# Kernel tuning notes

Hardware: AMD Instinct MI355X
Metric: run time of the kernel (lower is better)

The kernel has to match this reference:

```python
import jax, jax.numpy as jnp
import numpy as np

# SLAYER neuron / simulation constants (from params)
THETA = 10.0      # spike threshold
TAU_SR = 10.0     # PSP (synaptic response) time constant
TS = 1.0          # simulation time step
TAU_RHO = 1.0     # surrogate-gradient width
SCALE_RHO = 1.0   # surrogate-gradient scale
ALPHA = float(np.exp(-TS / TAU_SR))  # leaky-filter decay per step

B, C_IN, T = 32, 156, 2048
HID, OUT = 512, 20


@jax.custom_vjp
def spike(u):
    # Hard threshold with SLAYER-style exponential surrogate gradient.
    return (u >= THETA).astype(u.dtype)

def _spike_fwd(u):
    return spike(u), u

def _spike_bwd(u, g):
    sg = (SCALE_RHO / TAU_RHO) * jnp.exp(-jnp.abs(u - THETA) / TAU_RHO)
    return (g * sg,)

spike.defvjp(_spike_fwd, _spike_bwd)


def psp(x):
    # Leaky exponential temporal filter along the LAST axis (SLAYER psp):
    # y[t] = ALPHA * y[t-1] + x[t]
    xt = jnp.moveaxis(x, -1, 0)  # [T, ...]
    def step(c, xi):
        c = ALPHA * c + xi
        return c, c
    _, y = jax.lax.scan(step, jnp.zeros_like(xt[0]), xt)
    return jnp.moveaxis(y, 0, -1)


def dense(x, W):
    # SLAYER dense layer: per-timestep fully-connected over channel dim.
    # x: [N, C, H, W, T], W: [O, C] -> [N, O, H, W, T]
    return jnp.einsum('oc,nchwt->nohwt', W, x)


def _make_perm():
    rng = np.random.default_rng(0)
    random_list = rng.permutation(np.arange(1, 40))
    perm = []
    for i in random_list:
        perm.append(2 * int(i) - 2)
        perm.append(2 * int(i) - 1)
    for i in random_list:
        perm.append(2 * int(i) - 2 + 78)
        perm.append(2 * int(i) - 1 + 78)
    return jnp.asarray(perm, dtype=jnp.int32)


def setup_inputs() -> dict:
    key = jax.random.key(0)
    k0, k1, k2, k3, k4 = jax.random.split(key, 5)
    spike_input = jax.random.randint(k0, (B, C_IN, 1, 1, T), 0, 2).astype(jnp.float32)
    W1 = jax.random.normal(k1, (HID, C_IN), dtype=jnp.float32) * (C_IN ** -0.5)
    W2 = jax.random.normal(k2, (OUT, HID), dtype=jnp.float32) * (HID ** -0.5)
    Wl1 = jax.random.normal(k3, (HID, T), dtype=jnp.float32) * (T ** -0.5)
    Wl2 = jax.random.normal(k4, (OUT, HID), dtype=jnp.float32) * (HID ** -0.5)
    perm = _make_perm()
    return {"spike_input": spike_input, "W1": W1, "W2": W2,
            "Wl1": Wl1, "Wl2": Wl2, "perm": perm}


def reference(spike_input, W1, W2, Wl1, Wl2, perm):
    # Branch 1: channel-dense over taxels, PSP + spike, twice.
    s1 = spike(psp(dense(spike_input, W1)))          # [B, HID, 1, 1, T]
    spike_output = spike(psp(dense(s1, W2)))         # [B, OUT, 1, 1, T]

    # Branch 2: transpose channel<->time, permute taxel axis, dense over time dim.
    x_t = jnp.swapaxes(spike_input, 1, 4)            # [B, T, 1, 1, C_IN]
    x_tp = x_t[..., perm]                            # gather on taxel axis
    l1 = spike(psp(dense(x_tp, Wl1)))                # [B, HID, 1, 1, C_IN]
    location_output = spike(psp(dense(l1, Wl2)))     # [B, OUT, 1, 1, C_IN]

    return jnp.concatenate([spike_output, location_output], axis=4)
```

## Files before the change

kernel.cpp:

```cpp
#include <hip/hip_runtime.h>

#define ALPHA  0.90483741803595952f
#define ALPHA8 0.44932896411722156f
#define A64C   5.82e-23f
#define THETA  10.0f
#define BF1    ((unsigned short)0x3F80)
#define ISCALE 0.015625f

typedef short   bf16x8 __attribute__((ext_vector_type(8)));
typedef float   f32x4  __attribute__((ext_vector_type(4)));
typedef float   f32x4v __attribute__((ext_vector_type(4)));
typedef unsigned short ushort4v __attribute__((ext_vector_type(4)));
typedef unsigned short ushort8v __attribute__((ext_vector_type(8)));
typedef unsigned char  uchar4v  __attribute__((ext_vector_type(4)));
typedef unsigned char  uchar8v  __attribute__((ext_vector_type(8)));
typedef long long i64;

#define DMA16(gsrc, ldst)                                                     \
    __builtin_amdgcn_global_load_lds(                                         \
        (const __attribute__((address_space(1))) unsigned int*)(gsrc),        \
        (__attribute__((address_space(3))) unsigned int*)(ldst), 16, 0, 0)

__device__ __forceinline__ i64 tr16(const unsigned char* p) {
    i64 r;
    asm volatile("ds_read_b64_tr_b16 %0, %1"
                 : "=v"(r)
                 : "v"((const __attribute__((address_space(3))) unsigned char*)p));
    return r;
}

__device__ __forceinline__ unsigned short f2bf(float f) {
    unsigned int x = __float_as_uint(f);
    unsigned int r = (x + 0x7FFFu + ((x >> 16) & 1u)) >> 16;
    return (unsigned short)r;
}
__device__ __forceinline__ float bf2f(unsigned short h) {
    return __uint_as_float(((unsigned int)h) << 16);
}
__device__ __forceinline__ void split2(float w, unsigned short& h0,
                                       unsigned short& h1) {
    h0 = f2bf(w);          float r0 = w - bf2f(h0);
    h1 = f2bf(r0);
}
__device__ __forceinline__ unsigned char f2fp8(float f) {
    int pk = __builtin_amdgcn_cvt_pk_fp8_f32(f, 0.f, 0, false);
    return (unsigned char)(pk & 0xFF);
}
__device__ __forceinline__ float fp82f(unsigned char b) {
    return __builtin_amdgcn_cvt_f32_fp8((int)b, 0);
}

__global__ __launch_bounds__(256) void prep_scan_pack(
    const float* __restrict__ In, unsigned char* __restrict__ Infp8,
    unsigned short* __restrict__ Pbf,
    const float* __restrict__ W1,  const float* __restrict__ W2,
    const float* __restrict__ Wl1, const float* __restrict__ Wl2,
    unsigned short* __restrict__ W1p,  unsigned char* __restrict__ W2p8,
    unsigned char* __restrict__ Wl1p8, unsigned short* __restrict__ Wl2p)
{
    const int blk = blockIdx.x;
    const int tid = threadIdx.x;
    if (blk >= 6080) {
        int idx = blk - 6080;
        int b = idx >> 2, c = 156 + (idx & 3);
        ushort8v z = {0,0,0,0,0,0,0,0};
        *(ushort8v*)(Pbf + (long long)(b * 160 + c) * 2048 + tid * 8) = z;
        return;
    }
    if (blk < 1088) {
        if (blk < 512) {
            int m = blk;
            for (int k = tid; k < 2048; k += 256) {
                float w = Wl1[(long long)m * 2048 + k] * 64.0f;
                unsigned char h0 = f2fp8(w);
                unsigned char h1 = f2fp8(w - fp82f(h0));
                Wl1p8[(long long)m * 2048 + k] = h0;
                Wl1p8[1048576 + (long long)m * 2048 + k] = h1;
            }
        } else if (blk < 1024) {
            int m = blk - 512;
            for (int k = tid; k < 160; k += 256) {
                float v = (k < 156) ? W1[(long long)m * 156 + k] : 0.f;
                unsigned short h0, h1;
                split2(v, h0, h1);
                W1p[(long long)m * 160 + k] = h0;
                W1p[81920 + (long long)m * 160 + k] = h1;
            }
        } else if (blk < 1056) {
            int m = blk - 1024;
            for (int k = tid; k < 512; k += 256) {
                float w = (m < 20) ? W2[(long long)m * 512 + k] : 0.f;
                unsigned char h0 = f2fp8(w);
                unsigned char h1 = f2fp8(w - fp82f(h0));
                W2p8[(long long)m * 512 + k] = h0;
                W2p8[16384 + (long long)m * 512 + k] = h1;
            }
        } else {
            int m = blk - 1056;
            for (int k = tid; k < 512; k += 256) {
                float v = (m < 20) ? Wl2[(long long)m * 512 + k] : 0.f;
                unsigned short h0, h1;
                split2(v, h0, h1);
                Wl2p[(long long)m * 512 + k] = h0;
                Wl2p[16384 + (long long)m * 512 + k] = h1;
            }
        }
        return;
    }

    const int row = blk - 1088;
    const int bN  = row / 156;
    const int prow = bN * 160 + (row - bN * 156);
    const float* x = In + (long long)row * 2048 + tid * 8;
    const unsigned char ONE8 = f2fp8(1.0f);

    float v[8];
    *(f32x4v*)&v[0] = *(const f32x4v*)x;
    *(f32x4v*)&v[4] = *(const f32x4v*)(x + 4);

    uchar8v raw;
    #pragma unroll
    for (int k = 0; k < 8; ++k) raw[k] = (v[k] >= 0.5f) ? ONE8 : (unsigned char)0;
    *(uchar8v*)(Infp8 + (long long)row * 2048 + tid * 8) = raw;

    float y = 0.f;
    #pragma unroll
    for (int k = 0; k < 8; ++k) { y = ALPHA * y + v[k]; v[k] = y; }

    const int lane = tid & 63, wid = tid >> 6;
    float val = y, mm = ALPHA8;
    #pragma unroll
    for (int d = 1; d < 64; d <<= 1) {
        float p = __shfl_up(val, d);
        if (lane >= d) val += mm * p;
        mm *= mm;
    }
    __shared__ float wsum[4];
    if (lane == 63) wsum[wid] = val;
    __syncthreads();
    float pw = 0.f;
    #pragma unroll
    for (int w2 = 0; w2 < 3; ++w2)
        if (w2 < wid) pw = pw * A64C + wsum[w2];
    float prev = __shfl_up(val, 1);
    float a8l  = __expf(-0.8f * (float)lane);
    float carry = (lane == 0) ? pw : (prev + a8l * pw);

    ushort8v pv;
    float ak = ALPHA;
    #pragma unroll
    for (int k = 0; k < 8; ++k) {
        float yk = v[k] + ak * carry;
        ak *= ALPHA;
        pv[k] = f2bf(yk);
    }
    *(ushort8v*)(Pbf + (long long)prow * 2048 + tid * 8) = pv;
}

__global__ __launch_bounds__(256) void mega_gemm1(
    const unsigned short* __restrict__ W1p,
    const unsigned short* __restrict__ Pbf,
    unsigned short* __restrict__ S1bits,
    const unsigned char* __restrict__ Wl1p8,
    const unsigned char* __restrict__ Infp8,
    unsigned short* __restrict__ Zp)
{
    __shared__ alignas(16) unsigned char SMEM[49152];
    const int bx  = blockIdx.x;
    const int tid = threadIdx.x;
    const int lane = tid & 63, w = tid >> 6;
    const int wy = w >> 1, wx = w & 1;
    const int l15 = lane & 15, kq = lane >> 4;
    const int key = (l15 >> 1) & 3;

    if (bx >= 160) {
        unsigned char* Ab = SMEM;
        unsigned char* Bb = SMEM + 32768;

        const int id1 = bx - 160;
        const int z  = id1 >> 6;
        const int m0 = ((id1 >> 4) & 3) * 128;
        const int n0 = (id1 & 15) * 128;

        const unsigned short* gA[4]; int ldsA[4];
        #pragma unroll
        for (int s = 0; s < 4; ++s) {
            int id = tid + s * 256;
            int pl = id >> 9, m = (id >> 2) & 127, g = id & 3;
            int gs = g ^ ((m >> 1) & 3);
            gA[s] = W1p + (long long)pl * 81920 + (long long)(m0 + m) * 160 + gs * 8;
            ldsA[s] = id * 16;
        }
        const unsigned short* gB[2];
        #pragma unroll
        for (int s = 0; s < 2; ++s) {
            int id = tid + s * 256;
            int c  = ((id >> 6) << 2) | ((id >> 1) & 3);
            int t8 = ((((id >> 3) & 7) << 1) | (id & 1)) << 3;
            gB[s] = Pbf + (long long)(z * 160 + c) * 2048 + n0 + t8;
        }

        auto dmaA = [&](int buf) {
            unsigned char* dst = Ab + buf * 16384;
            #pragma unroll
            for (int s = 0; s < 4; ++s) { DMA16(gA[s], dst + ldsA[s]); gA[s] += 32; }
        };
        auto dmaB = [&](int buf) {
            unsigned char* dst = Bb + buf * 8192;
            #pragma unroll
            for (int s = 0; s < 2; ++s) {
                DMA16(gB[s], dst + (tid + s * 256) * 16);
                gB[s] += 65536;
            }
        };

        int aOff[2][4];
        #pragma unroll
        for (int pl = 0; pl < 2; ++pl)
            #pragma unroll
            for (int mt = 0; mt < 4; ++mt)
                aOff[pl][mt] = pl * 8192 + (wy * 64 + mt * 16 + l15) * 64 +
                               ((kq ^ key) * 16);
        const int bTr = wx * 512 + kq * 1920;

        f32x4 acc[4][4] = {};

        dmaA(0); dmaB(0);
        __syncthreads();

        #pragma unroll
        for (int it = 0; it < 5; ++it) {
            const int cur = it & 1;
            if (it < 4) { dmaA(cur ^ 1); dmaB(cur ^ 1); }

            const unsigned char* Ac = Ab + cur * 16384;
            const unsigned char* vB = Bb + cur * 8192 + bTr;
            bf16x8 bfr[4];
            #pragma unroll
            for (int nt = 0; nt < 4; ++nt) {
                union { i64 q[2]; bf16x8 v; } u;
                u.q[0] = tr16(vB + nt * 128);
                u.q[1] = tr16(vB + 1024 + nt * 128);
                bfr[nt] = u.v;
            }
            asm volatile("s_waitcnt lgkmcnt(0)" ::: "memory");
            __builtin_amdgcn_sched_barrier(0);

            #pragma unroll
            for (int pl = 0; pl < 2; ++pl) {
                #pragma unroll
                for (int mt = 0; mt < 4; ++mt) {
                    bf16x8 afr = *(const bf16x8*)(Ac + aOff[pl][mt]);
                    #pragma unroll
                    for (int nt = 0; nt < 4; ++nt)
                        acc[mt][nt] = __builtin_amdgcn_mfma_f32_16x16x32_bf16(
                            afr, bfr[nt], acc[mt][nt], 0, 0, 0);
                }
            }
            __syncthreads();
        }

        unsigned short* Db = S1bits + (long long)z * 512 * 128;
        #pragma unroll
        for (int mt = 0; mt < 4; ++mt) {
            #pragma unroll
            for (int i = 0; i < 4; ++i) {
                int m = m0 + wy * 64 + mt * 16 + kq * 4 + i;
                #pragma unroll
                for (int nt = 0; nt < 4; ++nt) {
                    unsigned long long mask = __ballot(acc[mt][nt][i] >= THETA);
                    if (l15 == 0) {
                        int nchunk = (n0 + wx * 64 + nt * 16) >> 4;
                        Db[(long long)nchunk * 512 + m] =
                            (unsigned short)((mask >> (kq * 16)) & 0xFFFFu);
                    }
                }
            }
        }
    } else {
        unsigned char* Ab = SMEM;
        unsigned char* Bb = SMEM + 32768;

        const int id0 = bx;
        const int nIdx = id0 % 40;
        if (nIdx >= 39) return;
        const int rest = id0 / 40;
        const int n0  = nIdx * 128;
        const int m0  = rest * 128;

        const unsigned char* gA8[4]; int ldsA8[4];
        #pragma unroll
        for (int s = 0; s < 4; ++s) {
            int id = tid + s * 256;
            int pl = id >> 9, m = (id >> 2) & 127, g = id & 3;
            int gs = g ^ ((m >> 1) & 3);
            gA8[s] = Wl1p8 + (long long)pl * 1048576 +
                     (long long)(m0 + m) * 2048 + gs * 16;
            ldsA8[s] = id * 16;
        }
        const unsigned char* gB8[2]; int ldsB8[2];
        #pragma unroll
        for (int s = 0; s < 2; ++s) {
            int id = tid + s * 256;
            int n = id >> 2, g = id & 3;
            int gs = g ^ ((n >> 1) & 3);
            gB8[s] = Infp8 + (long long)(n0 + n) * 2048 + gs * 16;
            ldsB8[s] = id * 16;
        }

        auto dmaA8 = [&](int buf) {
            unsigned char* dst = Ab + buf * 16384;
            #pragma unroll
            for (int s = 0; s < 4; ++s) { DMA16(gA8[s], dst + ldsA8[s]); gA8[s] += 64; }
        };
        auto dmaB8 = [&](int buf) {
            unsigned char* dst = Bb + buf * 8192;
            #pragma unroll
            for (int s = 0; s < 2; ++s) { DMA16(gB8[s], dst + ldsB8[s]); gB8[s] += 64; }
        };

        int aO8[2][4][2], bO8[4][2];
        #pragma unroll
        for (int ks = 0; ks < 2; ++ks) {
            const int gl = ks * 2 + (kq >> 1);
            const int sub = ((gl ^ key) * 16) + (kq & 1) * 8;
            #pragma unroll
            for (int pl = 0; pl < 2; ++pl)
                #pragma unroll
                for (int mt = 0; mt < 4; ++mt)
                    aO8[pl][mt][ks] = pl * 8192 +
                        (wy * 64 + mt * 16 + l15) * 64 + sub;
            #pragma unroll
            for (int nt = 0; nt < 4; ++nt)
                bO8[nt][ks] = (wx * 64 + nt * 16 + l15) * 64 + sub;
        }

        f32x4 acc[4][4] = {};

        dmaA8(0); dmaB8(0);
        __syncthreads();

        for (int it = 0; it < 32; ++it) {
            const int cur = it & 1;
            if (it < 31) { dmaA8(cur ^ 1); dmaB8(cur ^ 1); }

            const unsigned char* Ac = Ab + cur * 16384;
            const unsigned char* Bc = Bb + cur * 8192;
            #pragma unroll
            for (int ks = 0; ks < 2; ++ks) {
                i64 bfr[4];
                #pragma unroll
                for (int nt = 0; nt < 4; ++nt)
                    bfr[nt] = *(const i64*)(Bc + bO8[nt][ks]);
                #pragma unroll
                for (int pl = 0; pl < 2; ++pl) {
                    #pragma unroll
                    for (int mt = 0; mt < 4; ++mt) {
                        i64 afr = *(const i64*)(Ac + aO8[pl][mt][ks]);
                        #pragma unroll
                        for (int nt = 0; nt < 4; ++nt)
                            acc[mt][nt] = __builtin_amdgcn_mfma_f32_16x16x32_fp8_fp8(
                                afr, bfr[nt], acc[mt][nt], 0, 0, 0);
                    }
                }
            }
            __syncthreads();
        }

        unsigned short* Tu = (unsigned short*)SMEM;
        #pragma unroll
        for (int mt = 0; mt < 4; ++mt) {
            #pragma unroll
            for (int i = 0; i < 4; ++i) {
                int mL = wy * 64 + mt * 16 + kq * 4 + i;
                #pragma unroll
                for (int nt = 0; nt < 4; ++nt) {
                    int nL = wx * 64 + nt * 16 + l15;
                    Tu[mL * 130 + nL] = f2bf(acc[mt][nt][i] * ISCALE);
                }
            }
        }
        __syncthreads();

        #pragma unroll
        for (int s2 = 0; s2 < 64; ++s2) {
            int id = tid + s2 * 256;
            int cL = id >> 7;
            int mL = id & 127;
            int n = n0 + cL;
            int bb = n / 156, cc = n - bb * 156;
            Zp[(long long)cc * 16384 + bb * 512 + m0 + mL] = Tu[mL * 130 + cL];
        }
    }
}

__global__ __launch_bounds__(256) void mega_stage2(
    const unsigned char* __restrict__ W2p8,
    const unsigned short* __restrict__ S1bits,
    float* __restrict__ C2p,
    const unsigned short* __restrict__ Zp,
    const int* __restrict__ perm,
    unsigned short* __restrict__ L1T)
{
    __shared__ alignas(16) unsigned char SMEM[27648];
    const int bx  = blockIdx.x;
    const int tid = threadIdx.x;

    if (bx >= 512) {
        auto As = (unsigned char (*)[2][32][72])SMEM;
        auto Bs = (unsigned char (*)[128][72])(SMEM + 9216);

        const int bxg = bx - 512;
        const int lane = tid & 63, w = tid >> 6;
        const int l15 = lane & 15, kq = lane >> 4;
        const int n0  = (bxg & 15) * 128;
        const int b   = bxg >> 4;

        const unsigned short* Bb = S1bits + (long long)b * 512 * 128;
        const unsigned char ONE8 = f2fp8(1.0f);

        int aPl[2], aM[2], aK8[2];
        #pragma unroll
        for (int s = 0; s < 2; ++s) {
            int id = tid + s * 256;
            aPl[s] = id >> 8; int rem = id & 255;
            aM[s] = rem >> 3; aK8[s] = (rem & 7) * 8;
        }
        const int kb = (tid >> 4) * 4;
        const int nb = (tid & 15) * 8;
        const int nchunk = (n0 + nb) >> 4;
        const int nshift = nb & 15;

        f32x4 acc[2][2] = {};
        uchar8v aReg[2];
        unsigned short bBits[4];

        auto loadA = [&](int k0) {
            #pragma unroll
            for (int s = 0; s < 2; ++s)
                aReg[s] = *(const uchar8v*)(W2p8 + (long long)aPl[s] * 16384 +
                                            (long long)aM[s] * 512 + k0 + aK8[s]);
        };
        auto loadB = [&](int k0) {
            unsigned long long u = *(const unsigned long long*)
                (Bb + (long long)nchunk * 512 + k0 + kb);
            bBits[0] = (unsigned short)u;
            bBits[1] = (unsigned short)(u >> 16);
            bBits[2] = (unsigned short)(u >> 32);
            bBits[3] = (unsigned short)(u >> 48);
        };
        auto stage = [&](int buf) {
            #pragma unroll
            for (int s = 0; s < 2; ++s) *(uchar8v*)&As[buf][aPl[s]][aM[s]][aK8[s]] = aReg[s];
            unsigned char bv[4][8];
            #pragma unroll
            for (int kk2 = 0; kk2 < 4; ++kk2) {
                unsigned int bits = ((unsigned int)bBits[kk2] >> nshift) & 0xFFu;
                #pragma unroll
                for (int j = 0; j < 8; ++j)
                    bv[kk2][j] = ((bits >> j) & 1u) ? ONE8 : (unsigned char)0;
            }
            #pragma unroll
            for (int j = 0; j < 8; ++j) {
                uchar4v v4 = { bv[0][j], bv[1][j], bv[2][j], bv[3][j] };
                *(uchar4v*)&Bs[buf][nb + j][kb] = v4;
            }
        };

        loadA(0); loadB(0);
        stage(0);
        __syncthreads();

        #pragma unroll
        for (int it = 0; it < 8; ++it) {
            const int cur = it & 1;
            const int kn = (it + 1) * 64;
            if (it < 7) { loadA(kn); loadB(kn); }

            #pragma unroll
            for (int ks = 0; ks < 2; ++ks) {
                i64 bfr[2];
                #pragma unroll
                for (int nt = 0; nt < 2; ++nt)
                    bfr[nt] = *(const i64*)&Bs[cur][w * 32 + nt * 16 + l15][ks * 32 + kq * 8];
                #pragma unroll
                for (int pl = 0; pl < 2; ++pl) {
                    #pragma unroll
                    for (int mt = 0; mt < 2; ++mt) {
                        i64 afr = *(const i64*)&As[cur][pl][mt * 16 + l15][ks * 32 + kq * 8];
                        #pragma unroll
                        for (int nt = 0; nt < 2; ++nt)
                            acc[mt][nt] = __builtin_amdgcn_mfma_f32_16x16x32_fp8_fp8(
                                afr, bfr[nt], acc[mt][nt], 0, 0, 0);
                    }
                }
            }

            if (it < 7) stage(cur ^ 1);
            __syncthreads();
        }

        float* Cb = C2p + (long long)b * 20 * 2048;
        #pragma unroll
        for (int mt = 0; mt < 2; ++mt) {
            #pragma unroll
            for (int i = 0; i < 4; ++i) {
                int m = mt * 16 + kq * 4 + i;
                if (m >= 20) continue;
                #pragma unroll
                for (int nt = 0; nt < 2; ++nt) {
                    int n = n0 + w * 32 + nt * 16 + l15;
                    Cb[(long long)m * 2048 + n] = acc[mt][nt][i];
                }
            }
        }
    } else {
        auto Xs = (float (*)[32])SMEM;
        int* p  = (int*)(SMEM + 19968);

        const int r0 = bx * 32;
        for (int i = tid; i < 156; i += 256) p[i] = perm[i];

        const int row = tid & 31;
        const int cq  = tid >> 5;
        #pragma unroll
        for (int it = 0; it < 20; ++it) {
            int c = it * 8 + cq;
            if (c < 156) {
                Xs[c][row] = bf2f(Zp[(long long)c * 16384 + r0 + row]);
            }
        }
        __syncthreads();

        if (tid < 32) {
            float y = 0.f;
            for (int c = 0; c < 156; ++c) {
                y = ALPHA * y + Xs[p[c]][tid];
                L1T[(long long)c * 16384 + r0 + tid] = (y >= THETA) ? BF1 : 0;
            }
        }
    }
}

__global__ __launch_bounds__(256) void mega_stage3(
    const float* __restrict__ C2p, float* __restrict__ out,
    const unsigned short* __restrict__ Wl2p,
    const unsigned short* __restrict__ L1T)
{
    __shared__ alignas(16) unsigned char SMEM[36864];
    const int bx  = blockIdx.x;
    const int tid = threadIdx.x;

    if (bx >= 32) {
        const int row = bx - 32;
        const float* x = C2p + (long long)row * 2048 + tid * 8;

        float v[8];
        *(f32x4v*)&v[0] = *(const f32x4v*)x;
        *(f32x4v*)&v[4] = *(const f32x4v*)(x + 4);

        float y = 0.f;
        #pragma unroll
        for (int k = 0; k < 8; ++k) { y = ALPHA * y + v[k]; v[k] = y; }

        const int lane = tid & 63, wid = tid >> 6;
        float val = y, mm = ALPHA8;
        #pragma unroll
        for (int d = 1; d < 64; d <<= 1) {
            float p = __shfl_up(val, d);
            if (lane >= d) val += mm * p;
            mm *= mm;
        }
        float* wsum = (float*)SMEM;
        if (lane == 63) wsum[wid] = val;
        __syncthreads();
        float pw = 0.f;
        #pragma unroll
        for (int w2 = 0; w2 < 3; ++w2)
            if (w2 < wid) pw = pw * A64C + wsum[w2];
        float prev = __shfl_up(val, 1);
        float a8l  = __expf(-0.8f * (float)lane);
        float carry = (lane == 0) ? pw : (prev + a8l * pw);

        float* o = out + (long long)row * 2204 + tid * 8;
        float ak = ALPHA;
        #pragma unroll
        for (int k = 0; k < 8; ++k) {
            float yk = v[k] + ak * carry;
            ak *= ALPHA;
            o[k] = (yk >= THETA) ? 1.0f : 0.0f;
        }
    } else {
        auto As = (unsigned short (*)[32][72])SMEM;
        auto Bs = (unsigned short (*)[72])(SMEM + 9216);

        const int b  = bx;
        const int lane = tid & 63, w = tid >> 6;
        const int l15 = lane & 15, kq = lane >> 4;

        f32x4 acc[2][3] = {};

        for (int k0 = 0; k0 < 512; k0 += 64) {
            #pragma unroll
            for (int s = 0; s < 2; ++s) {
                int id = tid + s * 256;
                int pl = id >> 8, rem = id & 255;
                int m = rem >> 3, k8 = (rem & 7) * 8;
                ushort8v v = *(const ushort8v*)(Wl2p + (long long)pl * 16384 +
                                                (long long)m * 512 + k0 + k8);
                *(ushort8v*)&As[pl][m][k8] = v;
            }
            #pragma unroll
            for (int s = 0; s < 6; ++s) {
                int id = tid + s * 256;
                int n = id >> 3, k8 = (id & 7) * 8;
                ushort8v v = {0,0,0,0,0,0,0,0};
                if (n < 156)
                    v = *(const ushort8v*)(L1T + (long long)n * 16384 +
                                           b * 512 + k0 + k8);
                *(ushort8v*)&Bs[n][k8] = v;
            }
            __syncthreads();

            #pragma unroll
            for (int ks = 0; ks < 2; ++ks) {
                bf16x8 bfr[3];
                #pragma unroll
                for (int nt = 0; nt < 3; ++nt)
                    bfr[nt] = *(const bf16x8*)&Bs[w * 48 + nt * 16 + l15][ks * 32 + kq * 8];
                #pragma unroll
                for (int s = 0; s < 2; ++s) {
                    #pragma unroll
                    for (int mt = 0; mt < 2; ++mt) {
                        bf16x8 afr = *(const bf16x8*)&As[s][mt * 16 + l15][ks * 32 + kq * 8];
                        #pragma unroll
                        for (int nt = 0; nt < 3; ++nt)
                            acc[mt][nt] = __builtin_amdgcn_mfma_f32_16x16x32_bf16(
                                afr, bfr[nt], acc[mt][nt], 0, 0, 0);
                    }
                }
            }
            __syncthreads();
        }

        float* Cs = (float*)SMEM;
        #pragma unroll
        for (int mt = 0; mt < 2; ++mt) {
            #pragma unroll
            for (int i = 0; i < 4; ++i) {
                int m = mt * 16 + kq * 4 + i;
                #pragma unroll
                for (int nt = 0; nt < 3; ++nt) {
                    int n = w * 48 + nt * 16 + l15;
                    Cs[m * 193 + n] = acc[mt][nt][i];
                }
            }
        }
        __syncthreads();

        if (tid < 20) {
            const float* cr = Cs + tid * 193;
            float* o = out + (long long)(b * 20 + tid) * 2204 + 2048;
            float y = 0.f;
            for (int c = 0; c < 156; ++c) {
                y = ALPHA * y + cr[c];
                o[c] = (y >= THETA) ? 1.0f : 0.0f;
            }
        }
    }
}

extern "C" void kernel_launch(void* const* d_in, const int* in_sizes, int n_in,
                              void* d_out, int out_size, void* d_ws, size_t ws_size,
                              hipStream_t stream)
{
    const float* In  = (const float*)d_in[0];
    const float* W1  = (const float*)d_in[1];
    const float* W2  = (const float*)d_in[2];
    const float* Wl1 = (const float*)d_in[3];
    const float* Wl2 = (const float*)d_in[4];
    const int*  perm = (const int*)d_in[5];
    float* out = (float*)d_out;

    float* ws = (float*)d_ws;
    unsigned short* S1bits = (unsigned short*)ws;
    float* C2p = ws + 1048576LL;
    unsigned char*  Infp8 = (unsigned char*)(ws + 3670016LL);
    unsigned short* Pbf  = (unsigned short*)(ws + 6225920LL);
    unsigned short* W1p  = (unsigned short*)(ws + 16580608LL);
    unsigned char*  W2p8 = (unsigned char*)(ws + 16662528LL);
    unsigned char*  Wl1p8= (unsigned char*)(ws + 16670720LL);
    unsigned short* Wl2p = (unsigned short*)(ws + 17195008LL);
    unsigned short* Zpbf = (unsigned short*)(ws + 17211392LL);
    unsigned short* L1T  = (unsigned short*)(ws + 22323200LL);

    dim3 blk(256);

    prep_scan_pack<<<dim3(6208), blk, 0, stream>>>(
        In, Infp8, Pbf, W1, W2, Wl1, Wl2, W1p, W2p8, Wl1p8, Wl2p);

    mega_gemm1<<<dim3(2208), blk, 0, stream>>>(W1p, Pbf, S1bits,
                                               Wl1p8, Infp8, Zpbf);
    mega_stage2<<<dim3(1024), blk, 0, stream>>>(W2p8, S1bits, C2p,
                                                Zpbf, perm, L1T);
    mega_stage3<<<dim3(672), blk, 0, stream>>>(C2p, out, Wl2p, L1T);

    (void)in_sizes; (void)n_in; (void)out_size; (void)ws_size;
}
```

Measured before the change: 170.3 us.

## Triple-buffer fp8 location-branch GEMM with smaller K-steps and vmcnt waits

The location-branch fp8 GEMM moves from a double-buffered loop with 64-byte K chunks to a triple-buffered loop with 32-byte K chunks. It uses explicit s_waitcnt vmcnt and a raw s_barrier in place of a full __syncthreads per iteration, and raises wave priority around the MFMA block. The aim is to keep two loads in flight and hide global-to-LDS latency behind compute while shrinking the LDS footprint. The cost is twice as many barriers, and correctness depends on the hand-tuned vmcnt count and the new XOR swizzle matching.

```diff
diff --git a/kernel.cpp b/kernel.cpp
--- a/kernel.cpp
+++ b/kernel.cpp
@@ -279,7 +279,7 @@
         }
     } else {
         unsigned char* Ab = SMEM;
-        unsigned char* Bb = SMEM + 32768;
+        unsigned char* Bb = SMEM + 24576;
 
         const int id0 = bx;
         const int nIdx = id0 % 40;
@@ -288,84 +288,86 @@
         const int n0  = nIdx * 128;
         const int m0  = rest * 128;
 
-        const unsigned char* gA8[4]; int ldsA8[4];
-        #pragma unroll
-        for (int s = 0; s < 4; ++s) {
-            int id = tid + s * 256;
-            int pl = id >> 9, m = (id >> 2) & 127, g = id & 3;
-            int gs = g ^ ((m >> 1) & 3);
-            gA8[s] = Wl1p8 + (long long)pl * 1048576 +
-                     (long long)(m0 + m) * 2048 + gs * 16;
-            ldsA8[s] = id * 16;
-        }
-        const unsigned char* gB8[2]; int ldsB8[2];
+        const unsigned char* gA8[2]; int ldsA8[2];
         #pragma unroll
         for (int s = 0; s < 2; ++s) {
             int id = tid + s * 256;
-            int n = id >> 2, g = id & 3;
-            int gs = g ^ ((n >> 1) & 3);
-            gB8[s] = Infp8 + (long long)(n0 + n) * 2048 + gs * 16;
-            ldsB8[s] = id * 16;
+            int pl = id >> 8, m = (id >> 1) & 127, c = id & 1;
+            int src = (c * 16) ^ (((m >> 2) & 1) * 16);
+            gA8[s] = Wl1p8 + (long long)pl * 1048576 +
+                     (long long)(m0 + m) * 2048 + src;
+            ldsA8[s] = id * 16;
+        }
+        const unsigned char* gB8;
+        {
+            int id = tid;
+            int n = id >> 1, c = id & 1;
+            int src = (c * 16) ^ (((n >> 2) & 1) * 16);
+            gB8 = Infp8 + (long long)(n0 + n) * 2048 + src;
         }
 
         auto dmaA8 = [&](int buf) {
-            unsigned char* dst = Ab + buf * 16384;
-            #pragma unroll
-            for (int s = 0; s < 4; ++s) { DMA16(gA8[s], dst + ldsA8[s]); gA8[s] += 64; }
+            unsigned char* dst = Ab + buf * 8192;
+            #pragma unroll
+            for (int s = 0; s < 2; ++s) { DMA16(gA8[s], dst + ldsA8[s]); gA8[s] += 32; }
         };
         auto dmaB8 = [&](int buf) {
-            unsigned char* dst = Bb + buf * 8192;
-            #pragma unroll
-            for (int s = 0; s < 2; ++s) { DMA16(gB8[s], dst + ldsB8[s]); gB8[s] += 64; }
+            unsigned char* dst = Bb + buf * 4096;
+            DMA16(gB8, dst + tid * 16);
+            gB8 += 32;
         };
 
-        int aO8[2][4][2], bO8[4][2];
-        #pragma unroll
-        for (int ks = 0; ks < 2; ++ks) {
-            const int gl = ks * 2 + (kq >> 1);
-            const int sub = ((gl ^ key) * 16) + (kq & 1) * 8;
-            #pragma unroll
-            for (int pl = 0; pl < 2; ++pl)
-                #pragma unroll
-                for (int mt = 0; mt < 4; ++mt)
-                    aO8[pl][mt][ks] = pl * 8192 +
-                        (wy * 64 + mt * 16 + l15) * 64 + sub;
+        int aO8[2][4], bO8[4];
+        #pragma unroll
+        for (int pl = 0; pl < 2; ++pl)
+            #pragma unroll
+            for (int mt = 0; mt < 4; ++mt) {
+                int r = wy * 64 + mt * 16 + l15;
+                aO8[pl][mt] = pl * 4096 + r * 32 +
+                              ((kq ^ (((r >> 2) & 1) << 1)) * 8);
+            }
+        #pragma unroll
+        for (int nt = 0; nt < 4; ++nt) {
+            int r = wx * 64 + nt * 16 + l15;
+            bO8[nt] = r * 32 + ((kq ^ (((r >> 2) & 1) << 1)) * 8);
+        }
+
+        f32x4 acc[4][4] = {};
+
+        dmaA8(0); dmaB8(0);
+        dmaA8(1); dmaB8(1);
+
+        for (int it = 0; it < 64; ++it) {
+            if (it < 63) asm volatile("s_waitcnt vmcnt(3)" ::: "memory");
+            else         asm volatile("s_waitcnt vmcnt(0)" ::: "memory");
+            __builtin_amdgcn_s_barrier();
+            __builtin_amdgcn_sched_barrier(0);
+            if (it < 62) {
+                int nb = (it + 2) % 3;
+                dmaA8(nb); dmaB8(nb);
+            }
+
+            const unsigned char* Ac = Ab + (it % 3) * 8192;
+            const unsigned char* Bc = Bb + (it % 3) * 4096;
+            i64 bfr[4];
             #pragma unroll
             for (int nt = 0; nt < 4; ++nt)
-                bO8[nt][ks] = (wx * 64 + nt * 16 + l15) * 64 + sub;
-        }
-
-        f32x4 acc[4][4] = {};
-
-        dmaA8(0); dmaB8(0);
+                bfr[nt] = *(const i64*)(Bc + bO8[nt]);
+            __builtin_amdgcn_s_setprio(1);
+            #pragma unroll
+            for (int pl = 0; pl < 2; ++pl) {
+                #pragma unroll
+                for (int mt = 0; mt < 4; ++mt) {
+                    i64 afr = *(const i64*)(Ac + aO8[pl][mt]);
+                    #pragma unroll
+                    for (int nt = 0; nt < 4; ++nt)
+                        acc[mt][nt] = __builtin_amdgcn_mfma_f32_16x16x32_fp8_fp8(
+                            afr, bfr[nt], acc[mt][nt], 0, 0, 0);
+                }
+            }
+            __builtin_amdgcn_s_setprio(0);
+        }
         __syncthreads();
-
-        for (int it = 0; it < 32; ++it) {
-            const int cur = it & 1;
-            if (it < 31) { dmaA8(cur ^ 1); dmaB8(cur ^ 1); }
-
-            const unsigned char* Ac = Ab + cur * 16384;
-            const unsigned char* Bc = Bb + cur * 8192;
-            #pragma unroll
-            for (int ks = 0; ks < 2; ++ks) {
-                i64 bfr[4];
-                #pragma unroll
-                for (int nt = 0; nt < 4; ++nt)
-                    bfr[nt] = *(const i64*)(Bc + bO8[nt][ks]);
-                #pragma unroll
-                for (int pl = 0; pl < 2; ++pl) {
-                    #pragma unroll
-                    for (int mt = 0; mt < 4; ++mt) {
-                        i64 afr = *(const i64*)(Ac + aO8[pl][mt][ks]);
-                        #pragma unroll
-                        for (int nt = 0; nt < 4; ++nt)
-                            acc[mt][nt] = __builtin_amdgcn_mfma_f32_16x16x32_fp8_fp8(
-                                afr, bfr[nt], acc[mt][nt], 0, 0, 0);
-                    }
-                }
-            }
-            __syncthreads();
-        }
 
         unsigned short* Tu = (unsigned short*)SMEM;
         #pragma unroll
```

After: 171.8 us. No clear change (+0.9%).
